# Kernel tuning notes

Hardware: AMD Instinct MI355X
Metric: run time of the kernel (lower is better)

## Reference

```python
import jax, jax.numpy as jnp
import numpy as np

HEADS = 8  # diffusers default for hidden_size=320 (head_dim=40)


def setup_inputs() -> dict:
    key = jax.random.key(0)
    k0, k1, k2, k3, k4 = jax.random.split(key, 5)
    batches_of_frames, n, S, C = 1, 5, 1024, 320
    to_k_other = 2
    hidden_states = jax.random.normal(k0, (batches_of_frames * n, S, C), jnp.float32)
    Wq = jax.random.normal(k1, (C, C), jnp.float32) * 0.02
    Wk = jax.random.normal(k2, (C, C), jnp.float32) * 0.02
    Wv = jax.random.normal(k3, (C, C), jnp.float32) * 0.02
    Wo = jax.random.normal(k4, (C, C), jnp.float32) * 0.02
    bo = jnp.zeros((C,), jnp.float32)
    # set_config with random_others=False: self id first, then sequential others
    ids = np.array([[i] + [k for k in range(n) if k != i][:to_k_other] for i in range(n)], dtype=np.int64)
    return {"hidden_states": hidden_states, "Wq": Wq, "Wk": Wk, "Wv": Wv,
            "Wo": Wo, "bo": bo, "ids": jnp.asarray(ids)}


def reference(hidden_states, Wq, Wk, Wv, Wo, bo, ids):
    B, S, C = hidden_states.shape
    n, kf = ids.shape            # frames per group, selected frames per query frame
    Bf = B // n                  # batches_of_frames
    H = HEADS
    d = C // H

    q = hidden_states @ Wq                      # [B, S, C]
    k = hidden_states @ Wk
    v = hidden_states @ Wv

    def gather_frames(x):
        x = x.reshape(Bf, n, S, C)              # expand_batch
        x = x[:, ids]                           # [Bf, n, kf, S, C] cross-frame gather
        return x.reshape(Bf * n, kf * S, C)     # collapse_batch

    k = gather_frames(k)                        # [B, kf*S, C]
    v = gather_frames(v)

    q = q.reshape(B, S, H, d).transpose(0, 2, 1, 3)          # [B, H, S, d]
    k = k.reshape(B, kf * S, H, d).transpose(0, 2, 1, 3)     # [B, H, kf*S, d]
    v = v.reshape(B, kf * S, H, d).transpose(0, 2, 1, 3)

    scale = 1.0 / jnp.sqrt(jnp.asarray(d, q.dtype))
    scores = jnp.einsum('bhqd,bhkd->bhqk', q, k) * scale     # [B, H, S, kf*S]
    probs = jax.nn.softmax(scores, axis=-1)
    attn_out = jnp.einsum('bhqk,bhkd->bhqd', probs, v)       # [B, H, S, d]

    out = attn_out.transpose(0, 2, 1, 3).reshape(B, S, C)    # merge heads
    out = out @ Wo + bo                                      # to_out[0]; to_out[1] dropout = identity
    return out + hidden_states                               # residual, rescale_output_factor=1
```

## Files before the change

### kernel.cpp

```cpp
#include <hip/hip_runtime.h>
#include <hip/hip_bf16.h>

#define NB 5
#define NS 1024
#define NC 320
#define NH 8
#define ND 40
#define NKF 3
#define NBS (NB*NS)
#define NL (NKF*NS)
#define NCPAD 384
#define HP 48
#define QSTR 384

typedef __attribute__((ext_vector_type(4))) float f32x4;
typedef __attribute__((ext_vector_type(16))) float f32x16;
typedef __attribute__((ext_vector_type(8))) short bf16x8;
typedef __attribute__((ext_vector_type(4))) unsigned u32x4;

#define MFMA16(a,b,c) __builtin_amdgcn_mfma_f32_16x16x32_bf16((a),(b),(c),0,0,0)
#define MFMA32(a,b,c) __builtin_amdgcn_mfma_f32_32x32x16_bf16((a),(b),(c),0,0,0)

#define QSCALE 0.15811388300841898f

__device__ inline unsigned short f2bf(float f){
  unsigned int u = __builtin_bit_cast(unsigned int, f);
  u += 0x7fffu + ((u >> 16) & 1u);
  return (unsigned short)(u >> 16);
}

__device__ inline unsigned pkbf(float lo, float hi){
  unsigned r;
  asm("v_cvt_pk_bf16_f32 %0, %1, %2" : "=v"(r) : "v"(lo), "v"(hi));
  return r;
}

__global__ __launch_bounds__(256) void k_conv_hs(const float* __restrict__ hs,
                                                 unsigned short* __restrict__ hsb){
  int i = (blockIdx.x * 256 + threadIdx.x) * 4;
  float4 v = *(const float4*)&hs[i];
  ushort4 o;
  o.x = f2bf(v.x); o.y = f2bf(v.y); o.z = f2bf(v.z); o.w = f2bf(v.w);
  *(ushort4*)&hsb[i] = o;
}

__global__ void k_conv_w(const float* __restrict__ wq, const float* __restrict__ wk,
                         const float* __restrict__ wv, const float* __restrict__ wo,
                         unsigned short* __restrict__ wqT, unsigned short* __restrict__ wkT,
                         unsigned short* __restrict__ wvT, unsigned short* __restrict__ woT){
  int k = blockIdx.x * 16 + threadIdx.x;
  int n = blockIdx.y * 16 + threadIdx.y;
  const float* src; unsigned short* dst; float scl = 1.0f;
  switch (blockIdx.z){
    case 0: src = wq; dst = wqT; scl = QSCALE; break;
    case 1: src = wk; dst = wkT; break;
    case 2: src = wv; dst = wvT; break;
    default: src = wo; dst = woT; break;
  }
  dst[n*NC + k] = f2bf(src[k*NC + n] * scl);
}

__global__ __launch_bounds__(256) void k_zero_vtpad(unsigned short* __restrict__ vT){
  int i = blockIdx.x * 256 + threadIdx.x;
  bf16x8 z = {0,0,0,0,0,0,0,0};
  *(bf16x8*)&vT[(size_t)NC*NBS + (size_t)i*8] = z;
}

__global__ __launch_bounds__(256) void k_zero_qbpad(unsigned short* __restrict__ qbp){
  int t = blockIdx.x * 256 + threadIdx.x;
  int token = t >> 3, hh = t & 7;
  bf16x8 z = {0,0,0,0,0,0,0,0};
  *(bf16x8*)&qbp[token*QSTR + hh*HP + ND] = z;
}

__global__ __launch_bounds__(256) void k_qkv(const unsigned short* __restrict__ hsb,
    const unsigned short* __restrict__ wqT, const unsigned short* __restrict__ wkT,
    const unsigned short* __restrict__ wvT,
    unsigned short* __restrict__ qb, unsigned short* __restrict__ kb,
    unsigned short* __restrict__ vT){
  int wave = threadIdx.x >> 6, lane = threadIdx.x & 63;
  int lane16 = lane & 15, grp = lane >> 4;
  int m0 = blockIdx.x * 64, n0 = blockIdx.y * 64;
  int mat = blockIdx.z;
  const unsigned short* wT = (mat == 0) ? wqT : ((mat == 1) ? wkT : wvT);
  int arow = m0 + wave * 16 + lane16;
  f32x4 acc[4];
  #pragma unroll
  for (int t = 0; t < 4; t++) acc[t] = (f32x4){0.f,0.f,0.f,0.f};
  #pragma unroll
  for (int k0 = 0; k0 < NC; k0 += 32){
    bf16x8 a = *(const bf16x8*)&hsb[arow*NC + k0 + grp*8];
    #pragma unroll
    for (int t = 0; t < 4; t++){
      bf16x8 b = *(const bf16x8*)&wT[(n0 + t*16 + lane16)*NC + k0 + grp*8];
      acc[t] = MFMA16(a, b, acc[t]);
    }
  }
  int crow = m0 + wave * 16 + grp * 4;
  #pragma unroll
  for (int t = 0; t < 4; t++){
    int cc = n0 + t*16 + lane16;
    #pragma unroll
    for (int r = 0; r < 4; r++){
      unsigned short val = f2bf(acc[t][r]);
      int rr = crow + r;
      if (mat == 0){
        int hh = cc / ND, dd = cc - hh*ND;
        qb[rr*QSTR + hh*HP + dd] = val;
      } else if (mat == 1) kb[rr*NC + cc] = val;
      else                 vT[cc*NBS + rr] = val;
    }
  }
}

__global__ __launch_bounds__(192, 3) void k_attn(const unsigned short* __restrict__ qb,
    const unsigned short* __restrict__ kb, const unsigned short* __restrict__ vT,
    const int* __restrict__ ids, unsigned short* __restrict__ ao){
  __shared__ float ldsO[NKF][32][64];
  __shared__ float ldsM[NKF][32];
  __shared__ float ldsL[NKF][32];
  __shared__ float ldsCF[NKF][32];
  int w = threadIdx.x >> 6, lane = threadIdx.x & 63;
  int l31 = lane & 31, hi = lane >> 5;
  int b = blockIdx.z, h = blockIdx.y;
  int q0 = blockIdx.x * 32;
  int tokf = ids[b*NKF + w] * NS;

  bf16x8 qf0, qf1, qf2;
  {
    int qoff = (b*NS + q0 + l31) * QSTR + h*HP + hi*8;
    qf0 = *(const bf16x8*)&qb[qoff];
    qf1 = *(const bf16x8*)&qb[qoff + 16];
    qf2 = *(const bf16x8*)&qb[qoff + 32];
  }

  f32x16 o0, o1;
  #pragma unroll
  for (int r = 0; r < 16; r++){ o0[r] = 0.f; o1[r] = 0.f; }
  float m2 = -1e30f, lsum = 0.f;

  const int vrow0 = (h*ND + l31) * NBS + tokf;
  const int vrow1 = (h*ND + 32 + l31) * NBS + tokf;

  for (int kv = 0; kv < NS; kv += 32){
    int krow = (tokf + kv + l31)*NC + h*ND + hi*8;
    bf16x8 k0 = *(const bf16x8*)&kb[krow];
    bf16x8 k1 = *(const bf16x8*)&kb[krow + 16];
    bf16x8 k2 = *(const bf16x8*)&kb[krow + 32];
    bf16x8 v00 = *(const bf16x8*)&vT[vrow0 + kv + hi*8];
    bf16x8 v01 = *(const bf16x8*)&vT[vrow0 + kv + 16 + hi*8];
    bf16x8 v10 = *(const bf16x8*)&vT[vrow1 + kv + hi*8];
    bf16x8 v11 = *(const bf16x8*)&vT[vrow1 + kv + 16 + hi*8];

    f32x16 s;
    #pragma unroll
    for (int r = 0; r < 16; r++) s[r] = 0.f;
    s = MFMA32(k0, qf0, s);
    s = MFMA32(k1, qf1, s);
    s = MFMA32(k2, qf2, s);

    float t0 = fmaxf(fmaxf(s[0], s[1]), fmaxf(s[2], s[3]));
    float t1 = fmaxf(fmaxf(s[4], s[5]), fmaxf(s[6], s[7]));
    float t2 = fmaxf(fmaxf(s[8], s[9]), fmaxf(s[10], s[11]));
    float t3 = fmaxf(fmaxf(s[12], s[13]), fmaxf(s[14], s[15]));
    float pmax = fmaxf(fmaxf(t0, t1), fmaxf(t2, t3));
    pmax = fmaxf(pmax, __shfl_xor(pmax, 32));

    if (!__all(pmax - m2 <= 8.0f)){
      float mnew = fmaxf(m2, pmax);
      float cf = __expf(m2 - mnew);
      lsum *= cf;
      if (lane < 32) ldsCF[w][l31] = cf;
      #pragma unroll
      for (int r = 0; r < 16; r++){
        float c = ldsCF[w][(r&3) + 8*(r>>2) + 4*hi];
        o0[r] *= c; o1[r] *= c;
      }
      m2 = mnew;
    }

    float p[16];
    #pragma unroll
    for (int r = 0; r < 16; r++) p[r] = __expf(s[r] - m2);
    float a0 = (p[0]+p[1]) + (p[2]+p[3]);
    float a1 = (p[4]+p[5]) + (p[6]+p[7]);
    float a2 = (p[8]+p[9]) + (p[10]+p[11]);
    float a3 = (p[12]+p[13]) + (p[14]+p[15]);
    float ts = (a0+a1) + (a2+a3);
    ts += __shfl_xor(ts, 32);
    lsum += ts;

    u32x4 pw0, pw1;
    #pragma unroll
    for (int ks = 0; ks < 2; ks++){
      int qa = 2*ks + hi;
      int qp = 2*ks + 1 - hi;
      unsigned A0 = pkbf(p[4*qa+0], p[4*qa+1]);
      unsigned A1 = pkbf(p[4*qa+2], p[4*qa+3]);
      unsigned B0 = pkbf(p[4*qp+0], p[4*qp+1]);
      unsigned B1 = pkbf(p[4*qp+2], p[4*qp+3]);
      unsigned R0 = (unsigned)__shfl_xor((int)B0, 32);
      unsigned R1 = (unsigned)__shfl_xor((int)B1, 32);
      u32x4 wd;
      if (hi == 0){ wd[0]=A0; wd[1]=A1; wd[2]=R0; wd[3]=R1; }
      else        { wd[0]=R0; wd[1]=R1; wd[2]=A0; wd[3]=A1; }
      if (ks == 0) pw0 = wd; else pw1 = wd;
    }
    bf16x8 pa0 = __builtin_bit_cast(bf16x8, pw0);
    bf16x8 pa1 = __builtin_bit_cast(bf16x8, pw1);

    o0 = MFMA32(pa0, v00, o0);
    o0 = MFMA32(pa1, v01, o0);
    o1 = MFMA32(pa0, v10, o1);
    o1 = MFMA32(pa1, v11, o1);
  }

  #pragma unroll
  for (int r = 0; r < 16; r++){
    int qq = (r&3) + 8*(r>>2) + 4*hi;
    ldsO[w][qq][l31]      = o0[r];
    ldsO[w][qq][32 + l31] = o1[r];
  }
  if (lane < 32){ ldsM[w][l31] = m2; ldsL[w][l31] = lsum; }
  __syncthreads();

  for (int t = threadIdx.x; t < 32*ND; t += 192){
    int qq = t / ND, d = t - (t / ND) * ND;
    float mA = ldsM[0][qq], mB = ldsM[1][qq], mC = ldsM[2][qq];
    float M = fmaxf(mA, fmaxf(mB, mC));
    float eA = __expf(mA - M), eB = __expf(mB - M), eC = __expf(mC - M);
    float L = ldsL[0][qq]*eA + ldsL[1][qq]*eB + ldsL[2][qq]*eC;
    float O = ldsO[0][qq][d]*eA + ldsO[1][qq][d]*eB + ldsO[2][qq][d]*eC;
    ao[(size_t)(b*NS + q0 + qq)*NC + h*ND + d] = f2bf(O / L);
  }
}

__global__ __launch_bounds__(256) void k_out(const unsigned short* __restrict__ ao,
    const unsigned short* __restrict__ woT, const float* __restrict__ bo,
    const float* __restrict__ hs, float* __restrict__ out){
  int wave = threadIdx.x >> 6, lane = threadIdx.x & 63;
  int lane16 = lane & 15, grp = lane >> 4;
  int m0 = blockIdx.x * 64, n0 = blockIdx.y * 64;
  int arow = m0 + wave*16 + lane16;
  f32x4 acc[4];
  #pragma unroll
  for (int t = 0; t < 4; t++) acc[t] = (f32x4){0.f,0.f,0.f,0.f};
  #pragma unroll
  for (int k0 = 0; k0 < NC; k0 += 32){
    bf16x8 a = *(const bf16x8*)&ao[arow*NC + k0 + grp*8];
    #pragma unroll
    for (int t = 0; t < 4; t++){
      bf16x8 b = *(const bf16x8*)&woT[(n0 + t*16 + lane16)*NC + k0 + grp*8];
      acc[t] = MFMA16(a, b, acc[t]);
    }
  }
  int crow = m0 + wave*16 + grp*4;
  #pragma unroll
  for (int t = 0; t < 4; t++){
    int cc = n0 + t*16 + lane16;
    #pragma unroll
    for (int r = 0; r < 4; r++){
      int rr = crow + r;
      out[rr*NC + cc] = acc[t][r] + bo[cc] + hs[rr*NC + cc];
    }
  }
}

extern "C" void kernel_launch(void* const* d_in, const int* in_sizes, int n_in,
                              void* d_out, int out_size, void* d_ws, size_t ws_size,
                              hipStream_t stream){
  const float* hs = (const float*)d_in[0];
  const float* Wq = (const float*)d_in[1];
  const float* Wk = (const float*)d_in[2];
  const float* Wv = (const float*)d_in[3];
  const float* Wo = (const float*)d_in[4];
  const float* bo = (const float*)d_in[5];
  const int*  ids = (const int*)d_in[6];
  float* out = (float*)d_out;

  unsigned short* hsb = (unsigned short*)d_ws;
  unsigned short* wqT = hsb + (size_t)NBS*NC;
  unsigned short* wkT = wqT + (size_t)NC*NC;
  unsigned short* wvT = wkT + (size_t)NC*NC;
  unsigned short* woT = wvT + (size_t)NC*NC;
  unsigned short* qb  = woT + (size_t)NC*NC;
  unsigned short* kb  = qb  + (size_t)NBS*QSTR;
  unsigned short* vT  = kb  + (size_t)NBS*NC;
  unsigned short* ao  = vT  + (size_t)NCPAD*NBS;

  k_conv_hs<<<dim3(NBS*NC/1024), dim3(256), 0, stream>>>(hs, hsb);
  k_conv_w<<<dim3(NC/16, NC/16, 4), dim3(16,16), 0, stream>>>(Wq, Wk, Wv, Wo, wqT, wkT, wvT, woT);
  k_zero_vtpad<<<dim3((NCPAD-NC)*NBS/8/256), dim3(256), 0, stream>>>(vT);
  k_zero_qbpad<<<dim3(NBS*NH/256), dim3(256), 0, stream>>>(qb);
  k_qkv<<<dim3(NBS/64, NC/64, 3), dim3(256), 0, stream>>>(hsb, wqT, wkT, wvT, qb, kb, vT);
  k_attn<<<dim3(NS/32, NH, NB), dim3(192), 0, stream>>>(qb, kb, vT, ids, ao);
  k_out<<<dim3(NBS/64, NC/64, 1), dim3(256), 0, stream>>>(ao, woT, bo, hs, out);
}
```

Measured before the change: 287.3 us.

## Tile K/V per token-block and head, use exp2 with log2e folded into Q

The QKV kernel now writes K and V into contiguous per-(32-token block, head) tiles, so each attention iteration reads compact, coalesced chunks instead of strided rows across the full token dimension. The softmax switches to raw v_exp_f32 (base 2), with log2(e) folded into the Q weight scale. The separate V padding zero-fill kernel is removed, and the attention output buffer now reuses the bf16 hidden-state buffer. The risk is that the K tile padding (columns 40-47) is never written, so uninitialised workspace bytes could inject NaN or Inf through the zero-padded Q product.

Result: faster. 274.8 us (-4.4%).

```diff
diff --git a/kernel.cpp b/kernel.cpp
--- a/kernel.cpp
+++ b/kernel.cpp
@@ -9,9 +9,10 @@
 #define NKF 3
 #define NBS (NB*NS)
 #define NL (NKF*NS)
-#define NCPAD 384
 #define HP 48
 #define QSTR 384
+#define KTILE (32*48)
+#define VTILE (64*32)
 
 typedef __attribute__((ext_vector_type(4))) float f32x4;
 typedef __attribute__((ext_vector_type(16))) float f32x16;
@@ -21,7 +22,13 @@
 #define MFMA16(a,b,c) __builtin_amdgcn_mfma_f32_16x16x32_bf16((a),(b),(c),0,0,0)
 #define MFMA32(a,b,c) __builtin_amdgcn_mfma_f32_32x32x16_bf16((a),(b),(c),0,0,0)
 
-#define QSCALE 0.15811388300841898f
+#define QSCALE2 0.22811012f
+
+__device__ inline float ex2(float x){
+  float r;
+  asm("v_exp_f32 %0, %1" : "=v"(r) : "v"(x));
+  return r;
+}
 
 __device__ inline unsigned short f2bf(float f){
   unsigned int u = __builtin_bit_cast(unsigned int, f);
@@ -52,18 +59,12 @@
   int n = blockIdx.y * 16 + threadIdx.y;
   const float* src; unsigned short* dst; float scl = 1.0f;
   switch (blockIdx.z){
-    case 0: src = wq; dst = wqT; scl = QSCALE; break;
+    case 0: src = wq; dst = wqT; scl = QSCALE2; break;
     case 1: src = wk; dst = wkT; break;
     case 2: src = wv; dst = wvT; break;
     default: src = wo; dst = woT; break;
   }
   dst[n*NC + k] = f2bf(src[k*NC + n] * scl);
-}
-
-__global__ __launch_bounds__(256) void k_zero_vtpad(unsigned short* __restrict__ vT){
-  int i = blockIdx.x * 256 + threadIdx.x;
-  bf16x8 z = {0,0,0,0,0,0,0,0};
-  *(bf16x8*)&vT[(size_t)NC*NBS + (size_t)i*8] = z;
 }
 
 __global__ __launch_bounds__(256) void k_zero_qbpad(unsigned short* __restrict__ qbp){
@@ -100,15 +101,15 @@
   #pragma unroll
   for (int t = 0; t < 4; t++){
     int cc = n0 + t*16 + lane16;
+    int hh = cc / ND, dd = cc - hh*ND;
     #pragma unroll
     for (int r = 0; r < 4; r++){
       unsigned short val = f2bf(acc[t][r]);
       int rr = crow + r;
-      if (mat == 0){
-        int hh = cc / ND, dd = cc - hh*ND;
-        qb[rr*QSTR + hh*HP + dd] = val;
-      } else if (mat == 1) kb[rr*NC + cc] = val;
-      else                 vT[cc*NBS + rr] = val;
+      int tokblk = rr >> 5, tl = rr & 31;
+      if (mat == 0)      qb[rr*QSTR + hh*HP + dd] = val;
+      else if (mat == 1) kb[(((size_t)tokblk*NH + hh)*32 + tl)*HP + dd] = val;
+      else               vT[(((size_t)tokblk*NH + hh)*64 + dd)*32 + tl] = val;
     }
   }
 }
@@ -124,7 +125,7 @@
   int l31 = lane & 31, hi = lane >> 5;
   int b = blockIdx.z, h = blockIdx.y;
   int q0 = blockIdx.x * 32;
-  int tokf = ids[b*NKF + w] * NS;
+  int frame = ids[b*NKF + w];
 
   bf16x8 qf0, qf1, qf2;
   {
@@ -134,41 +135,42 @@
     qf2 = *(const bf16x8*)&qb[qoff + 32];
   }
 
+  const unsigned short* kbase = kb + ((size_t)(frame*32)*NH + h)*KTILE + l31*HP + hi*8;
+  const unsigned short* vbase = vT + ((size_t)(frame*32)*NH + h)*VTILE + l31*32 + hi*8;
+
   f32x16 o0, o1;
   #pragma unroll
   for (int r = 0; r < 16; r++){ o0[r] = 0.f; o1[r] = 0.f; }
+  const f32x16 z16 = o0;
   float m2 = -1e30f, lsum = 0.f;
 
-  const int vrow0 = (h*ND + l31) * NBS + tokf;
-  const int vrow1 = (h*ND + 32 + l31) * NBS + tokf;
-
-  for (int kv = 0; kv < NS; kv += 32){
-    int krow = (tokf + kv + l31)*NC + h*ND + hi*8;
-    bf16x8 k0 = *(const bf16x8*)&kb[krow];
-    bf16x8 k1 = *(const bf16x8*)&kb[krow + 16];
-    bf16x8 k2 = *(const bf16x8*)&kb[krow + 32];
-    bf16x8 v00 = *(const bf16x8*)&vT[vrow0 + kv + hi*8];
-    bf16x8 v01 = *(const bf16x8*)&vT[vrow0 + kv + 16 + hi*8];
-    bf16x8 v10 = *(const bf16x8*)&vT[vrow1 + kv + hi*8];
-    bf16x8 v11 = *(const bf16x8*)&vT[vrow1 + kv + 16 + hi*8];
-
-    f32x16 s;
-    #pragma unroll
-    for (int r = 0; r < 16; r++) s[r] = 0.f;
-    s = MFMA32(k0, qf0, s);
+  #pragma unroll 2
+  for (int kvb = 0; kvb < NS/32; kvb++){
+    const unsigned short* kp = kbase + (size_t)kvb * (NH*KTILE);
+    const unsigned short* vp = vbase + (size_t)kvb * (NH*VTILE);
+    bf16x8 k0 = *(const bf16x8*)(kp);
+    bf16x8 k1 = *(const bf16x8*)(kp + 16);
+    bf16x8 k2 = *(const bf16x8*)(kp + 32);
+    bf16x8 v00 = *(const bf16x8*)(vp);
+    bf16x8 v01 = *(const bf16x8*)(vp + 16);
+    bf16x8 v10 = *(const bf16x8*)(vp + 32*32);
+    bf16x8 v11 = *(const bf16x8*)(vp + 32*32 + 16);
+
+    f32x16 s = MFMA32(k0, qf0, z16);
     s = MFMA32(k1, qf1, s);
     s = MFMA32(k2, qf2, s);
 
-    float t0 = fmaxf(fmaxf(s[0], s[1]), fmaxf(s[2], s[3]));
-    float t1 = fmaxf(fmaxf(s[4], s[5]), fmaxf(s[6], s[7]));
-    float t2 = fmaxf(fmaxf(s[8], s[9]), fmaxf(s[10], s[11]));
-    float t3 = fmaxf(fmaxf(s[12], s[13]), fmaxf(s[14], s[15]));
-    float pmax = fmaxf(fmaxf(t0, t1), fmaxf(t2, t3));
+    float t0 = fmaxf(fmaxf(s[0], s[1]), s[2]);
+    float t1 = fmaxf(fmaxf(s[3], s[4]), s[5]);
+    float t2 = fmaxf(fmaxf(s[6], s[7]), s[8]);
+    float t3 = fmaxf(fmaxf(s[9], s[10]), s[11]);
+    float t4 = fmaxf(fmaxf(s[12], s[13]), s[14]);
+    float pmax = fmaxf(fmaxf(fmaxf(t0, t1), fmaxf(t2, t3)), fmaxf(t4, s[15]));
     pmax = fmaxf(pmax, __shfl_xor(pmax, 32));
 
     if (!__all(pmax - m2 <= 8.0f)){
       float mnew = fmaxf(m2, pmax);
-      float cf = __expf(m2 - mnew);
+      float cf = ex2(m2 - mnew);
       lsum *= cf;
       if (lane < 32) ldsCF[w][l31] = cf;
       #pragma unroll
@@ -181,7 +183,7 @@
 
     float p[16];
     #pragma unroll
-    for (int r = 0; r < 16; r++) p[r] = __expf(s[r] - m2);
+    for (int r = 0; r < 16; r++) p[r] = ex2(s[r] - m2);
     float a0 = (p[0]+p[1]) + (p[2]+p[3]);
     float a1 = (p[4]+p[5]) + (p[6]+p[7]);
     float a2 = (p[8]+p[9]) + (p[10]+p[11]);
@@ -227,8 +229,8 @@
   for (int t = threadIdx.x; t < 32*ND; t += 192){
     int qq = t / ND, d = t - (t / ND) * ND;
     float mA = ldsM[0][qq], mB = ldsM[1][qq], mC = ldsM[2][qq];
-    float M = fmaxf(mA, fmaxf(mB, mC));
-    float eA = __expf(mA - M), eB = __expf(mB - M), eC = __expf(mC - M);
+    float M = fmaxf(fmaxf(mA, mB), mC);
+    float eA = ex2(mA - M), eB = ex2(mB - M), eC = ex2(mC - M);
     float L = ldsL[0][qq]*eA + ldsL[1][qq]*eB + ldsL[2][qq]*eC;
     float O = ldsO[0][qq][d]*eA + ldsO[1][qq][d]*eB + ldsO[2][qq][d]*eC;
     ao[(size_t)(b*NS + q0 + qq)*NC + h*ND + d] = f2bf(O / L);
@@ -285,12 +287,11 @@
   unsigned short* woT = wvT + (size_t)NC*NC;
   unsigned short* qb  = woT + (size_t)NC*NC;
   unsigned short* kb  = qb  + (size_t)NBS*QSTR;
-  unsigned short* vT  = kb  + (size_t)NBS*NC;
-  unsigned short* ao  = vT  + (size_t)NCPAD*NBS;
+  unsigned short* vT  = kb  + (size_t)(NBS/32)*NH*KTILE;
+  unsigned short* ao  = hsb;
 
   k_conv_hs<<<dim3(NBS*NC/1024), dim3(256), 0, stream>>>(hs, hsb);
   k_conv_w<<<dim3(NC/16, NC/16, 4), dim3(16,16), 0, stream>>>(Wq, Wk, Wv, Wo, wqT, wkT, wvT, woT);
-  k_zero_vtpad<<<dim3((NCPAD-NC)*NBS/8/256), dim3(256), 0, stream>>>(vT);
   k_zero_qbpad<<<dim3(NBS*NH/256), dim3(256), 0, stream>>>(qb);
   k_qkv<<<dim3(NBS/64, NC/64, 3), dim3(256), 0, stream>>>(hsb, wqT, wkT, wvT, qb, kb, vT);
   k_attn<<<dim3(NS/32, NH, NB), dim3(192), 0, stream>>>(qb, kb, vT, ids, ao);
```
